# Performance work log

Measured on AMD Instinct MI355X. Metric: run time of the kernel, lower is better.

The kernel has to match this reference:

```python
import jax, jax.numpy as jnp
import numpy as np

EPS_BN = 1e-5

def _grid_sample(fea, gx, gy):
    # fea: [B,C,H,W]; gx,gy: [B,P] normalized to [-1,1]; bilinear, zeros padding, align_corners=True
    B, C, H, W = fea.shape
    x = (gx + 1.0) * 0.5 * (W - 1)
    y = (gy + 1.0) * 0.5 * (H - 1)
    x0 = jnp.floor(x)
    y0 = jnp.floor(y)
    wx1 = x - x0
    wy1 = y - y0
    flat = fea.reshape(B, C, H * W)
    def tap(xi, yi, w):
        valid = ((xi >= 0) & (xi <= W - 1) & (yi >= 0) & (yi <= H - 1)).astype(fea.dtype)
        xi_c = jnp.clip(xi, 0, W - 1).astype(jnp.int32)
        yi_c = jnp.clip(yi, 0, H - 1).astype(jnp.int32)
        g = jnp.take_along_axis(flat, (yi_c * W + xi_c)[:, None, :], axis=2)  # [B,C,P]
        return g * (w * valid)[:, None, :]
    return (tap(x0, y0, (1 - wx1) * (1 - wy1)) + tap(x0 + 1, y0, wx1 * (1 - wy1))
            + tap(x0, y0 + 1, (1 - wx1) * wy1) + tap(x0 + 1, y0 + 1, wx1 * wy1))

def _homo_warp(src_fea, src_proj, ref_proj, depth_values):
    # src_fea: [B,C,H,W] -> warped [B,C,D,H,W] (MVSNet homo_warping, grid under stop_gradient)
    B, C, H, W = src_fea.shape
    D = depth_values.shape[1]
    proj = jnp.matmul(src_proj, jnp.linalg.inv(ref_proj))
    rot, trans = proj[:, :3, :3], proj[:, :3, 3]
    yy, xx = jnp.meshgrid(jnp.arange(H, dtype=src_fea.dtype), jnp.arange(W, dtype=src_fea.dtype), indexing='ij')
    xyz = jnp.stack([xx.ravel(), yy.ravel(), jnp.ones(H * W, src_fea.dtype)], 0)  # [3,HW]
    rot_xyz = jnp.einsum('bij,jp->bip', rot, xyz)  # [B,3,HW]
    pxyz = rot_xyz[:, :, None, :] * depth_values.reshape(B, 1, D, H * W) + trans[:, :, None, None]  # [B,3,D,HW]
    z = pxyz[:, 2]
    gx = jax.lax.stop_gradient(((pxyz[:, 0] / z) / ((W - 1) / 2.0) - 1.0).reshape(B, D * H * W))
    gy = jax.lax.stop_gradient(((pxyz[:, 1] / z) / ((H - 1) / 2.0) - 1.0).reshape(B, D * H * W))
    return _grid_sample(src_fea, gx, gy).reshape(B, C, D, H, W)

def _pixelwise_net(x, w0, g0, b0, m0, v0, w1, g1, b1, m1, v1, w2, b2):
    # x: [B,1,D,H,W]; 1x1x1 Conv3d(bias=False)+BN+ReLU twice, then Conv3d(8->1)+sigmoid+max over D
    def bnrelu(h, g, b, m, v):
        s = (1, -1, 1, 1, 1)
        return jax.nn.relu((h - m.reshape(s)) * (g / jnp.sqrt(v + EPS_BN)).reshape(s) + b.reshape(s))
    h = bnrelu(jnp.einsum('oc,bcdhw->bodhw', w0, x), g0, b0, m0, v0)
    h = bnrelu(jnp.einsum('oc,bcdhw->bodhw', w1, h), g1, b1, m1, v1)
    h = jnp.einsum('oc,bcdhw->bodhw', w2, h) + b2.reshape(1, -1, 1, 1, 1)
    out = jax.nn.sigmoid(h[:, 0])  # [B,D,H,W]
    return jnp.max(out, axis=1, keepdims=True)  # [B,1,H,W]

def _forward(features, proj_matrices, depth_values, num_depth,
             pw_w0, pw_g0, pw_b0, pw_m0, pw_v0, pw_w1, pw_g1, pw_b1, pw_m1, pw_v1, pw_w2, pw_b2,
             reg_w, reg_b):
    ref_fea = features[0]
    B, C, H, W = ref_fea.shape
    V = features.shape[0]
    D = num_depth
    def proj_new(p):  # p: [B,2,4,4] -> K @ E on top 3 rows
        top = jnp.matmul(p[:, 1, :3, :3], p[:, 0, :3, :4])
        return jnp.concatenate([top, p[:, 0, 3:4, :]], axis=1)
    ref_proj_new = proj_new(proj_matrices[:, 0])
    sim_sum = jnp.zeros((B, 1, D, H, W), ref_fea.dtype)
    w_sum = jnp.full((B, 1, 1, H, W), 1e-5, ref_fea.dtype)
    vw_list = []
    for i in range(1, V):  # small fixed loop over source views
        src_proj_new = proj_new(proj_matrices[:, i])
        warped = _homo_warp(features[i], src_proj_new, ref_proj_new, depth_values)
        sim = jnp.mean(warped * ref_fea[:, :, None], axis=1, keepdims=True)  # [B,1,D,H,W]
        vw = _pixelwise_net(sim, pw_w0, pw_g0, pw_b0, pw_m0, pw_v0, pw_w1, pw_g1, pw_b1, pw_m1, pw_v1, pw_w2, pw_b2)
        vw_list.append(vw)
        sim_sum = sim_sum + sim * vw[:, :, None]
        w_sum = w_sum + vw[:, :, None]
    similarity = sim_sum / w_sum
    cost_reg = jax.lax.conv_general_dilated(similarity, reg_w, (1, 1, 1), 'SAME',
                                            dimension_numbers=('NCDHW', 'OIDHW', 'NCDHW')) + reg_b.reshape(1, -1, 1, 1, 1)
    prob_volume = jax.nn.softmax(cost_reg[:, 0], axis=1)  # exp(log_softmax) == softmax
    idx = jnp.argmax(prob_volume, axis=1, keepdims=True)
    depth = jnp.take_along_axis(depth_values, idx, axis=1)[:, 0]  # WTA depth [B,H,W]
    conf = jnp.max(prob_volume, axis=1)
    view_weights = jnp.concatenate(vw_list, axis=1)
    return depth, conf, prob_volume, cost_reg, view_weights

def setup_inputs():
    key = jax.random.key(0)
    ks = jax.random.split(key, 20)
    B, V, C, H, W, D = 2, 5, 32, 128, 160, 32
    features = jax.random.normal(ks[0], (V, B, C, H, W), jnp.float32)
    K = np.eye(4, dtype=np.float32)
    K[0, 0] = 180.0; K[1, 1] = 180.0; K[0, 2] = W / 2.0; K[1, 2] = H / 2.0
    pm = np.zeros((B, V, 2, 4, 4), np.float32)
    for v in range(V):
        E = np.eye(4, dtype=np.float32)
        E[0, 3] = 10.0 * v  # horizontal baseline per source view
        pm[:, v, 0] = E
        pm[:, v, 1] = K
    depth_values = jnp.broadcast_to(jnp.linspace(425.0, 935.0, D, dtype=jnp.float32)[None, :, None, None], (B, D, H, W)) + 0.0
    rn = lambda k, s, sc=0.3: jax.random.normal(k, s, jnp.float32) * sc
    return {
        'features': features,
        'proj_matrices': jnp.asarray(pm),
        'depth_values': depth_values,
        'num_depth': D,
        'pw_w0': rn(ks[1], (16, 1)),
        'pw_g0': 1.0 + rn(ks[2], (16,), 0.1), 'pw_b0': rn(ks[3], (16,), 0.1),
        'pw_m0': rn(ks[4], (16,), 0.1), 'pw_v0': 1.0 + 0.5 * jax.random.uniform(ks[5], (16,)),
        'pw_w1': rn(ks[6], (8, 16)),
        'pw_g1': 1.0 + rn(ks[7], (8,), 0.1), 'pw_b1': rn(ks[8], (8,), 0.1),
        'pw_m1': rn(ks[9], (8,), 0.1), 'pw_v1': 1.0 + 0.5 * jax.random.uniform(ks[10], (8,)),
        'pw_w2': rn(ks[11], (1, 8)),
        'pw_b2': rn(ks[12], (1,), 0.1),
        'reg_w': rn(ks[13], (1, 1, 3, 3, 3), 0.1),
        'reg_b': rn(ks[14], (1,), 0.1),
    }

def reference(features, proj_matrices, depth_values, num_depth,
              pw_w0, pw_g0, pw_b0, pw_m0, pw_v0, pw_w1, pw_g1, pw_b1, pw_m1, pw_v1, pw_w2, pw_b2,
              reg_w, reg_b):
    return _forward(features, proj_matrices, depth_values, num_depth,
                    pw_w0, pw_g0, pw_b0, pw_m0, pw_v0, pw_w1, pw_g1, pw_b1, pw_m1, pw_v1, pw_w2, pw_b2,
                    reg_w, reg_b)
```

## Files before the change

kernel.cpp:

```cpp
#include <hip/hip_runtime.h>
#include <math.h>

#define BB 2
#define VV 5
#define CC 32
#define HH 128
#define WW 160
#define DD 32
#define HWp (HH*WW)
#define NV (VV-1)
#define PX 16
#define MAXSLOT 18

#define OFF_RT   0
#define OFF_PRM  96
#define OFF_FEAT 512
#define OFF_SIM  (OFF_FEAT + VV*BB*HWp*CC)
#define OFF_T    (OFF_SIM + BB*DD*HWp)
#define OFF_TAB  (OFF_T + 16)
#define OFF_FLAG (OFF_TAB + 17*16)

#define OUT_DEPTH 0
#define OUT_CONF  (BB*HWp)
#define OUT_PROB  (2*BB*HWp)
#define OUT_COST  (OUT_PROB + BB*DD*HWp)
#define OUT_VW    (OUT_COST + BB*DD*HWp)

#define ZI(d,k)     smemU[(d)*17 + (k)]
#define DEP(d,k)    smemU[(d)*17 + (k)]
#define REF(p,c)    smemU[544 + (p)*36 + (c)]
#define GT(v,p,i)   smemU[1120 + ((v)*16 + (p))*18 + (i)]
#define AY0(v,p)    smemU[2272 + (v)*16 + (p)]
#define AY1(v,p)    smemU[2336 + (v)*16 + (p)]
#define IR0(v,p)    smemI[2400 + (v)*16 + (p)]
#define IR1(v,p)    smemI[2464 + (v)*16 + (p)]
#define IXB(v,p)    smemI[2528 + (v)*16 + (p)]
#define ISL(v,p)    smemI[2592 + (v)*16 + (p)]
#define BADF        smemI[2656]
#define SIMG(v,d,p) smemU[544 + (((v)*32 + (d))*17 + (p))]

__device__ void build_proj(const float* proj, int b, int v, double M[4][4]) {
    const float* E = proj + (((b*VV + v)*2 + 0)*16);
    const float* K = proj + (((b*VV + v)*2 + 1)*16);
    for (int r = 0; r < 3; r++)
        for (int c = 0; c < 4; c++) {
            double s = 0.0;
            for (int k = 0; k < 3; k++) s += (double)K[r*4+k] * (double)E[k*4+c];
            M[r][c] = s;
        }
    for (int c = 0; c < 4; c++) M[3][c] = (double)E[12+c];
}

__device__ void inv4(const double M[4][4], double out[4][4]) {
    double a[4][8];
    for (int i = 0; i < 4; i++)
        for (int j = 0; j < 4; j++) { a[i][j] = M[i][j]; a[i][4+j] = (i == j) ? 1.0 : 0.0; }
    for (int col = 0; col < 4; col++) {
        int piv = col; double best = fabs(a[col][col]);
        for (int r = col+1; r < 4; r++) if (fabs(a[r][col]) > best) { best = fabs(a[r][col]); piv = r; }
        if (piv != col) for (int j = 0; j < 8; j++) { double t = a[col][j]; a[col][j] = a[piv][j]; a[piv][j] = t; }
        double dinv = 1.0 / a[col][col];
        for (int j = 0; j < 8; j++) a[col][j] *= dinv;
        for (int r = 0; r < 4; r++) {
            if (r == col) continue;
            double f = a[r][col];
            for (int j = 0; j < 8; j++) a[r][j] -= f * a[col][j];
        }
    }
    for (int i = 0; i < 4; i++) for (int j = 0; j < 4; j++) out[i][j] = a[i][4+j];
}

__device__ void setup_body(const float* __restrict__ proj,
    const float* __restrict__ w0, const float* __restrict__ g0, const float* __restrict__ b0,
    const float* __restrict__ m0, const float* __restrict__ v0,
    const float* __restrict__ w1, const float* __restrict__ g1, const float* __restrict__ b1,
    const float* __restrict__ m1, const float* __restrict__ v1,
    const float* __restrict__ w2, const float* __restrict__ b2,
    float* __restrict__ ws, int t,
    float* __restrict__ prmL, float* __restrict__ TL) {

    if (t < BB*NV) {
        int b = t / NV, v = 1 + (t % NV);
        double refM[4][4], inv[4][4], S[4][4];
        build_proj(proj, b, 0, refM);
        inv4(refM, inv);
        build_proj(proj, b, v, S);
        float* rt = ws + OFF_RT + (b*NV + (v-1))*12;
        for (int r = 0; r < 3; r++) {
            for (int c = 0; c < 3; c++) {
                double s = 0.0;
                for (int k = 0; k < 4; k++) s += S[r][k] * inv[k][c];
                rt[r*3 + c] = (float)s;
            }
            double s = 0.0;
            for (int k = 0; k < 4; k++) s += S[r][k] * inv[k][3];
            rt[9 + r] = (float)s;
        }
    }

    if (t < 16) {
        float sc = g0[t] / sqrtf(v0[t] + 1e-5f);
        prmL[t]      = w0[t] * sc;
        prmL[16 + t] = b0[t] - m0[t] * sc;
    }
    if (t >= 32 && t < 160) {
        int i = t - 32, q = i >> 4, o = i & 15;
        float sc = g1[q] / sqrtf(v1[q] + 1e-5f);
        prmL[32 + q*16 + o] = w1[q*16 + o] * sc;
    }
    if (t >= 160 && t < 168) {
        int q = t - 160;
        float sc = g1[q] / sqrtf(v1[q] + 1e-5f);
        prmL[160 + q] = b1[q] - m1[q] * sc;
        prmL[168 + q] = w2[q];
    }
    if (t == 176) prmL[176] = b2[0];
    __syncthreads();

    if (t < BB) {
        int ok = 1;
        for (int i = 0; i < NV; i++) {
            const float* ri = ws + OFF_RT + (t*NV + i)*12;
            ok &= (fabsf(ri[6])        < 1e-6f);
            ok &= (fabsf(ri[7])        < 1e-6f);
            ok &= (fabsf(ri[8] - 1.f)  < 1e-6f);
            ok &= (fabsf(ri[10])       < 1e-6f);
            ok &= (fabsf(ri[11])       < 1e-6f);
        }
        ws[OFF_FLAG + t] = ok ? 1.f : 0.f;
    }

    if (t == 0) {
        float tmp[16]; int nk = 0;
        for (int o = 0; o < 16; o++) {
            float a = prmL[o];
            if (a != 0.f) tmp[nk++] = -prmL[16+o] / a;
        }
        for (int i = 1; i < nk; i++) {
            float key = tmp[i]; int j = i-1;
            while (j >= 0 && tmp[j] > key) { tmp[j+1] = tmp[j]; j--; }
            tmp[j+1] = key;
        }
        for (int i = 0; i < 16; i++) TL[i] = (i < nk) ? tmp[i] : 3.4e38f;
    }
    __syncthreads();

    if (t < 17*8) {
        int seg = t >> 3, q = t & 7;
        float lo = (seg == 0)  ? -1e30f : TL[seg-1];
        float hi = (seg == 16) ?  1e30f : TL[seg];
        float smid;
        if (hi > 1e29f)       smid = lo + 1.f;
        else if (lo < -1e29f) smid = hi - 1.f;
        else                  smid = 0.5f*(lo + hi);
        float alpha = 0.f, beta = prmL[160+q];
        #pragma unroll
        for (int o = 0; o < 16; o++) {
            float a = prmL[o], c = prmL[16+o];
            if (a*smid + c > 0.f) {
                alpha += prmL[32+q*16+o]*a;
                beta  += prmL[32+q*16+o]*c;
            }
        }
        ws[OFF_TAB + seg*16 + q]     = alpha;
        ws[OFF_TAB + seg*16 + 8 + q] = beta;
    }
    if (t < 177) ws[OFF_PRM + t] = prmL[t];
    if (t < 16)  ws[OFF_T + t]   = TL[t];
}

__global__ __launch_bounds__(256) void transpose_setup_kernel(
    const float* __restrict__ fea, float* __restrict__ featT,
    const float* __restrict__ proj,
    const float* __restrict__ w0, const float* __restrict__ g0, const float* __restrict__ b0,
    const float* __restrict__ m0, const float* __restrict__ v0,
    const float* __restrict__ w1, const float* __restrict__ g1, const float* __restrict__ b1,
    const float* __restrict__ m1, const float* __restrict__ v1,
    const float* __restrict__ w2, const float* __restrict__ b2,
    float* __restrict__ ws) {
    __shared__ float prmL[177];
    __shared__ float TL[16];
    if (blockIdx.x == 0)
        setup_body(proj, w0, g0, b0, m0, v0, w1, g1, b1, m1, v1, w2, b2,
                   ws, threadIdx.x, prmL, TL);

    int t = blockIdx.x*256 + threadIdx.x;
    int w = t % WW;
    int h = (t / WW) % HH;
    int b = (t / (WW*HH)) % BB;
    int v = t / (WW*HH*BB);
    const float* src = fea + (size_t)((v*BB + b)*CC) * HWp + h*WW + w;
    float* dst = featT + (size_t)((v*BB + b)*HWp + h*WW + w) * CC;
    #pragma unroll
    for (int c = 0; c < CC; c += 4) {
        float4 q;
        q.x = src[(c+0)*HWp];
        q.y = src[(c+1)*HWp];
        q.z = src[(c+2)*HWp];
        q.w = src[(c+3)*HWp];
        *reinterpret_cast<float4*>(dst + c) = q;
    }
}

__device__ __forceinline__ float half_max(float v) {
    v = fmaxf(v, __shfl_xor(v, 1));
    v = fmaxf(v, __shfl_xor(v, 2));
    v = fmaxf(v, __shfl_xor(v, 4));
    v = fmaxf(v, __shfl_xor(v, 8));
    v = fmaxf(v, __shfl_xor(v, 16));
    return v;
}

__device__ __forceinline__ float dot32(const float* __restrict__ col,
                                       const float* __restrict__ refp) {
    float acc = 0.f;
    #pragma unroll
    for (int c = 0; c < CC; c += 4) {
        float4 a = *reinterpret_cast<const float4*>(col + c);
        float4 r = *reinterpret_cast<const float4*>(refp + c);
        acc = fmaf(a.w, r.w, fmaf(a.z, r.z, fmaf(a.y, r.y, fmaf(a.x, r.x, acc))));
    }
    return acc;
}

__device__ __forceinline__ void mlp_out(
    float s0, float s1, float s2, float s3,
    int d2, int b, int p,
    const float* __restrict__ tabL, const float* __restrict__ Tg,
    const float* __restrict__ prm,
    float* __restrict__ out, float* __restrict__ simout) {
    float T0 = Tg[0], T1 = Tg[1], T2 = Tg[2], T3 = Tg[3];
    float T4 = Tg[4], T5 = Tg[5], T6 = Tg[6], T7 = Tg[7];
    float T8 = Tg[8], T9 = Tg[9], T10 = Tg[10], T11 = Tg[11];
    float T12 = Tg[12], T13 = Tg[13], T14 = Tg[14], T15 = Tg[15];
    float wq0 = prm[168], wq1 = prm[169], wq2 = prm[170], wq3 = prm[171];
    float wq4 = prm[172], wq5 = prm[173], wq6 = prm[174], wq7 = prm[175];
    float p176 = prm[176];

    float sv[NV] = {s0, s1, s2, s3};
    float vw[NV];
    #pragma unroll
    for (int v = 0; v < NV; v++) {
        float s = sv[v];
        int seg = 0;
        seg += (s > T0);  seg += (s > T1);  seg += (s > T2);  seg += (s > T3);
        seg += (s > T4);  seg += (s > T5);  seg += (s > T6);  seg += (s > T7);
        seg += (s > T8);  seg += (s > T9);  seg += (s > T10); seg += (s > T11);
        seg += (s > T12); seg += (s > T13); seg += (s > T14); seg += (s > T15);
        const float* row = &tabL[seg << 4];
        float4 A0 = *reinterpret_cast<const float4*>(row);
        float4 A1 = *reinterpret_cast<const float4*>(row + 4);
        float4 B0 = *reinterpret_cast<const float4*>(row + 8);
        float4 B1 = *reinterpret_cast<const float4*>(row + 12);
        float h2v = p176;
        h2v = fmaf(wq0, fmaxf(fmaf(A0.x, s, B0.x), 0.f), h2v);
        h2v = fmaf(wq1, fmaxf(fmaf(A0.y, s, B0.y), 0.f), h2v);
        h2v = fmaf(wq2, fmaxf(fmaf(A0.z, s, B0.z), 0.f), h2v);
        h2v = fmaf(wq3, fmaxf(fmaf(A0.w, s, B0.w), 0.f), h2v);
        h2v = fmaf(wq4, fmaxf(fmaf(A1.x, s, B1.x), 0.f), h2v);
        h2v = fmaf(wq5, fmaxf(fmaf(A1.y, s, B1.y), 0.f), h2v);
        h2v = fmaf(wq6, fmaxf(fmaf(A1.z, s, B1.z), 0.f), h2v);
        h2v = fmaf(wq7, fmaxf(fmaf(A1.w, s, B1.w), 0.f), h2v);
        float m = half_max(h2v);
        vw[v] = 1.f/(1.f + __expf(-m));
    }

    if (d2 == 0) out[OUT_VW + (b*NV + 0)*HWp + p] = vw[0];
    if (d2 == 1) out[OUT_VW + (b*NV + 1)*HWp + p] = vw[1];
    if (d2 == 2) out[OUT_VW + (b*NV + 2)*HWp + p] = vw[2];
    if (d2 == 3) out[OUT_VW + (b*NV + 3)*HWp + p] = vw[3];

    float wsum = 1e-5f + vw[0] + vw[1] + vw[2] + vw[3];
    float ssum = s0*vw[0] + s1*vw[1] + s2*vw[2] + s3*vw[3];
    simout[(b*DD + d2)*HWp + p] = ssum / wsum;
}

__device__ __forceinline__ float tap_blend(
    const float* __restrict__ vbv, int sub8, float sx,
    float ay0, float ay1, int r0, int r1,
    float4 rva, float4 rvb) {
    float x0f = floorf(sx);
    float wx1 = sx - x0f;
    float wx0 = 1.f - wx1;
    int xi0 = (int)x0f, xi1 = xi0 + 1;
    float ax0 = ((unsigned)xi0 < WW) ? wx0 : 0.f;
    float ax1 = ((unsigned)xi1 < WW) ? wx1 : 0.f;
    int xc0 = min(max(xi0, 0), WW-1);
    int xc1 = min(max(xi1, 0), WW-1);
    float w00 = ax0*ay0, w01 = ax1*ay0;
    const float* q00 = vbv + (((r0 + xc0) << 5) + sub8);
    const float* q01 = vbv + (((r0 + xc1) << 5) + sub8);
    float4 t00a = *reinterpret_cast<const float4*>(q00);
    float4 t00b = *reinterpret_cast<const float4*>(q00 + 4);
    float4 t01a = *reinterpret_cast<const float4*>(q01);
    float4 t01b = *reinterpret_cast<const float4*>(q01 + 4);

    float blx = fmaf(w01, t01a.x, w00*t00a.x);
    float bly = fmaf(w01, t01a.y, w00*t00a.y);
    float blz = fmaf(w01, t01a.z, w00*t00a.z);
    float blw = fmaf(w01, t01a.w, w00*t00a.w);
    float acc = fmaf(rva.w,blw, fmaf(rva.z,blz, fmaf(rva.y,bly, rva.x*blx)));
    blx = fmaf(w01, t01b.x, w00*t00b.x);
    bly = fmaf(w01, t01b.y, w00*t00b.y);
    blz = fmaf(w01, t01b.z, w00*t00b.z);
    blw = fmaf(w01, t01b.w, w00*t00b.w);
    acc = fmaf(rvb.w,blw, fmaf(rvb.z,blz, fmaf(rvb.y,bly, fmaf(rvb.x,blx, acc))));

    if (ay1 != 0.f) {
        float w10 = ax0*ay1, w11 = ax1*ay1;
        const float* q10 = vbv + (((r1 + xc0) << 5) + sub8);
        const float* q11 = vbv + (((r1 + xc1) << 5) + sub8);
        float4 t10a = *reinterpret_cast<const float4*>(q10);
        float4 t10b = *reinterpret_cast<const float4*>(q10 + 4);
        float4 t11a = *reinterpret_cast<const float4*>(q11);
        float4 t11b = *reinterpret_cast<const float4*>(q11 + 4);
        float cx = fmaf(w11, t11a.x, w10*t10a.x);
        float cy = fmaf(w11, t11a.y, w10*t10a.y);
        float cz = fmaf(w11, t11a.z, w10*t10a.z);
        float cw = fmaf(w11, t11a.w, w10*t10a.w);
        acc = fmaf(rva.w,cw, fmaf(rva.z,cz, fmaf(rva.y,cy, fmaf(rva.x,cx, acc))));
        cx = fmaf(w11, t11b.x, w10*t10b.x);
        cy = fmaf(w11, t11b.y, w10*t10b.y);
        cz = fmaf(w11, t11b.z, w10*t10b.z);
        cw = fmaf(w11, t11b.w, w10*t10b.w);
        acc = fmaf(rvb.w,cw, fmaf(rvb.z,cz, fmaf(rvb.y,cy, fmaf(rvb.x,cx, acc))));
    }
    return acc;
}

__global__ __launch_bounds__(256) void fused_sim_kernel(
    const float* __restrict__ featT, const float* __restrict__ rtAll,
    const float* __restrict__ prm, const float* __restrict__ Tg,
    const float* __restrict__ tabG, const float* __restrict__ flagG,
    const float* __restrict__ depthv,
    float* __restrict__ simout, float* __restrict__ out) {
    __shared__ __align__(16) float smemU[2720];
    __shared__ __align__(16) float tabL[17*16];
    int* smemI = (int*)smemU;

    int t = threadIdx.x;
    int b = blockIdx.y;
    int pbase = blockIdx.x * PX;
    int hi  = pbase / WW;
    int wi0 = pbase % WW;
    float fy = (float)hi;

    bool fast = (flagG[b] != 0.f);

    {
        int di = t >> 4, k = t & 15;
        float dep0 = depthv[(b*DD + di)*HWp + pbase + k];
        float dep1 = depthv[(b*DD + di + 16)*HWp + pbase + k];
        if (fast) {
            ZI(di, k)    = __builtin_amdgcn_rcpf(dep0);
            ZI(di+16, k) = __builtin_amdgcn_rcpf(dep1);
            REF(di, k)      = featT[(size_t)(b*HWp + pbase + di)*CC + k];
            REF(di, k+16)   = featT[(size_t)(b*HWp + pbase + di)*CC + k + 16];
        } else {
            DEP(di, k)    = dep0;
            DEP(di+16, k) = dep1;
        }
        tabL[t] = tabG[t];
        if (t < 16) tabL[256 + t] = tabG[256 + t];
        if (t == 0 && fast) BADF = 0;
    }
    __syncthreads();

    float rc[NV][12];
    #pragma unroll
    for (int v = 0; v < NV; v++)
        #pragma unroll
        for (int j = 0; j < 12; j++)
            rc[v][j] = rtAll[(b*NV + v)*12 + j];
    float bx0[NV], by0[NV], bz0[NV];
    #pragma unroll
    for (int v = 0; v < NV; v++) {
        bx0[v] = fmaf((float)wi0, rc[v][0], fmaf(fy, rc[v][1], rc[v][2]));
        by0[v] = fmaf((float)wi0, rc[v][3], fmaf(fy, rc[v][4], rc[v][5]));
        bz0[v] = fmaf((float)wi0, rc[v][6], fmaf(fy, rc[v][7], rc[v][8]));
    }

    bool needRestage = false;
    if (fast) {
        int p_loc = t >> 5, d = t & 31;
        for (int ph = 0; ph < 2; ph++) {
            int p = ph*8 + p_loc;
            float fk = (float)p;
            float zi = ZI(d, p);
            #pragma unroll
            for (int v = 0; v < NV; v++) {
                float bx = fmaf(fk, rc[v][0], bx0[v]);
                float sx = fmaf(rc[v][9], zi, bx);
                float mn = sx, mx = sx;
                #pragma unroll
                for (int off = 1; off <= 16; off <<= 1) {
                    mn = fminf(mn, __shfl_xor(mn, off));
                    mx = fmaxf(mx, __shfl_xor(mx, off));
                }
                if (d == 0) {
                    float by = fmaf(fk, rc[v][3], by0[v]);
                    float sy = by;
                    float sny = rintf(sy);
                    sy = (fabsf(sy - sny) < 1e-4f) ? sny : sy;
                    float y0f = floorf(sy);
                    float wy1 = sy - y0f, wy0 = 1.f - wy1;
                    int yi0 = (int)y0f, yi1 = yi0 + 1;
                    AY0(v, p) = ((unsigned)yi0 < HH) ? wy0 : 0.f;
                    AY1(v, p) = ((unsigned)yi1 < HH) ? wy1 : 0.f;
                    IR0(v, p) = min(max(yi0, 0), HH-1)*WW;
                    IR1(v, p) = min(max(yi1, 0), HH-1)*WW;
                    bool finite = (mn > -1e9f) && (mx < 1e9f) && (mn == mn) && (mx == mx);
                    int xb = finite ? (int)floorf(mn) : 0;
                    int slots = finite ? ((int)floorf(mx) - xb + 2) : MAXSLOT + 1;
                    IXB(v, p) = xb;
                    ISL(v, p) = slots;
                    if (slots > MAXSLOT) BADF = 1;
                }
            }
        }
        __syncthreads();
        if (BADF) { fast = false; needRestage = true; }
    }

    if (fast) {
        {
            int v2 = t & 3, p2 = (t >> 2) & 15, i0 = t >> 6;
            float ay0 = AY0(v2, p2), ay1 = AY1(v2, p2);
            int r0 = IR0(v2, p2), r1 = IR1(v2, p2);
            int xb = IXB(v2, p2), slots = ISL(v2, p2);
            const float* vbv = featT + (size_t)(((v2+1)*BB + b)*HWp)*CC;
            const float* refp = &REF(p2, 0);
            for (int i2 = i0; i2 < slots; i2 += 4) {
                int xc = min(max(xb + i2, 0), WW-1);
                float g = ay0 * dot32(vbv + ((r0 + xc) << 5), refp);
                if (ay1 != 0.f) g = fmaf(ay1, dot32(vbv + ((r1 + xc) << 5), refp), g);
                GT(v2, p2, i2) = g * (1.f/(float)CC);
            }
        }
        __syncthreads();
        {
            int p_loc = t >> 5, d = t & 31;
            for (int ph = 0; ph < 2; ph++) {
                int p = ph*8 + p_loc;
                float fk = (float)p;
                float zi = ZI(d, p);
                float sv[NV];
                #pragma unroll
                for (int v = 0; v < NV; v++) {
                    float bx = fmaf(fk, rc[v][0], bx0[v]);
                    float sx = fmaf(rc[v][9], zi, bx);
                    float x0f = floorf(sx);
                    float wx1 = sx - x0f, wx0 = 1.f - wx1;
                    int xi0 = (int)x0f, xi1 = xi0 + 1;
                    float ax0 = ((unsigned)xi0 < WW) ? wx0 : 0.f;
                    float ax1 = ((unsigned)xi1 < WW) ? wx1 : 0.f;
                    int ii = xi0 - IXB(v, p);
                    float g0 = GT(v, p, ii);
                    float g1 = GT(v, p, ii+1);
                    sv[v] = fmaf(ax0, g0, ax1*g1);
                }
                mlp_out(sv[0], sv[1], sv[2], sv[3], d, b, pbase + p,
                        tabL, Tg, prm, out, simout);
            }
        }
        return;
    }

    if (needRestage) {
        int di = t >> 4, k = t & 15;
        DEP(di, k)    = depthv[(b*DD + di)*HWp + pbase + k];
        DEP(di+16, k) = depthv[(b*DD + di + 16)*HWp + pbase + k];
        __syncthreads();
    }
    {
        int sub = t & 3;
        int dB  = (t >> 2) & 31;
        int kk  = t >> 7;
        int sub8 = sub*8;
        #pragma unroll 2
        for (int j = 0; j < PX/2; j++) {
            int kpix = j*2 + kk;
            int p = pbase + kpix;
            float fk = (float)kpix;
            float depth = DEP(dB, kpix);
            const float* refp = featT + (size_t)(b*HWp + p)*CC + sub8;
            float4 rva = *reinterpret_cast<const float4*>(refp);
            float4 rvb = *reinterpret_cast<const float4*>(refp + 4);

            #pragma unroll
            for (int v = 0; v < NV; v++) {
                float bx = fmaf(fk, rc[v][0], bx0[v]);
                float by = fmaf(fk, rc[v][3], by0[v]);
                float bz = fmaf(fk, rc[v][6], bz0[v]);
                float px = fmaf(bx, depth, rc[v][9]);
                float py = fmaf(by, depth, rc[v][10]);
                float pz = fmaf(bz, depth, rc[v][11]);
                float zi = __builtin_amdgcn_rcpf(pz);
                float sx = px * zi, sy = py * zi;
                float sny = rintf(sy);
                sy = (fabsf(sy - sny) < 1e-4f) ? sny : sy;
                float y0f = floorf(sy);
                float wy1 = sy - y0f, wy0 = 1.f - wy1;
                int yi0 = (int)y0f, yi1 = yi0 + 1;
                float ay0 = ((unsigned)yi0 < HH) ? wy0 : 0.f;
                float ay1 = ((unsigned)yi1 < HH) ? wy1 : 0.f;
                int yc0 = min(max(yi0, 0), HH-1);
                int yc1 = min(max(yi1, 0), HH-1);
                int r0 = yc0*WW, r1 = yc1*WW;
                const float* vbv = featT + (size_t)(((v+1)*BB + b)*HWp)*CC;
                float acc = tap_blend(vbv, sub8, sx, ay0, ay1, r0, r1, rva, rvb);
                acc += __shfl_xor(acc, 1);
                acc += __shfl_xor(acc, 2);
                if (sub == 0) SIMG(v, dB, kpix) = acc * (1.f/(float)CC);
            }
        }
        __syncthreads();

        int p8 = t >> 5;
        int d2 = t & 31;
        #pragma unroll
        for (int pi = 0; pi < PX/8; pi++) {
            int pidx = pi*8 + p8;
            mlp_out(SIMG(0, d2, pidx), SIMG(1, d2, pidx),
                    SIMG(2, d2, pidx), SIMG(3, d2, pidx),
                    d2, b, pbase + pidx, tabL, Tg, prm, out, simout);
        }
    }
}

__global__ __launch_bounds__(256) void convsm_kernel(
    const float* __restrict__ sim, const float* __restrict__ rw,
    const float* __restrict__ rb, const float* __restrict__ depthv,
    float* __restrict__ out) {
    __shared__ float tile[34*121 + 7];
    int t = threadIdx.x;
    int tw = blockIdx.x * 8;
    int th = blockIdx.y * 8;
    int b  = blockIdx.z;

    for (int i = t; i < 34*120; i += 256) {
        int e = i / 120; int rem = i % 120;
        int h = rem / 12, w = rem % 12;
        int gd = e - 1, gh = th + h - 1, gw = tw + w - 1;
        float v = 0.f;
        if (w < 10 && gd >= 0 && gd < DD && (unsigned)gh < HH && (unsigned)gw < WW)
            v = sim[((b*DD + gd)*HH + gh)*WW + gw];
        tile[e*121 + rem] = v;
    }
    __syncthreads();

    float wk[27];
    #pragma unroll
    for (int i = 0; i < 27; i++) wk[i] = rw[i];
    float bias = rb[0];

    int p  = t >> 2, dq = t & 3;
    int ph = p >> 3, pw = p & 7;
    int d0 = dq * 8;

    float cost[8];
    #pragma unroll
    for (int j = 0; j < 8; j++) cost[j] = bias;
    #pragma unroll
    for (int e = 0; e < 10; e++) {
        int el = d0 + e;
        float s0 = 0.f, s1 = 0.f, s2 = 0.f;
        #pragma unroll
        for (int kh = 0; kh < 3; kh++) {
            #pragma unroll
            for (int kw = 0; kw < 3; kw++) {
                float x = tile[el*121 + (ph+kh)*12 + (pw+kw)];
                s0 = fmaf(wk[0*9 + kh*3 + kw], x, s0);
                s1 = fmaf(wk[1*9 + kh*3 + kw], x, s1);
                s2 = fmaf(wk[2*9 + kh*3 + kw], x, s2);
            }
        }
        if (e < 8)            cost[e]   += s0;
        if (e >= 1 && e <= 8) cost[e-1] += s1;
        if (e >= 2)           cost[e-2] += s2;
    }

    int pg = (th + ph)*WW + (tw + pw);
    #pragma unroll
    for (int j = 0; j < 8; j++)
        out[OUT_COST + (b*DD + d0 + j)*HWp + pg] = cost[j];

    float m = cost[0]; int mi = d0;
    #pragma unroll
    for (int j = 1; j < 8; j++) { if (cost[j] > m) { m = cost[j]; mi = d0 + j; } }
    #pragma unroll
    for (int off = 1; off <= 2; off <<= 1) {
        float m2 = __shfl_xor(m, off);
        int  i2 = __shfl_xor(mi, off);
        if (m2 > m || (m2 == m && i2 < mi)) { m = m2; mi = i2; }
    }
    float sum = 0.f;
    float e8[8];
    #pragma unroll
    for (int j = 0; j < 8; j++) { e8[j] = __expf(cost[j] - m); sum += e8[j]; }
    #pragma unroll
    for (int off = 1; off <= 2; off <<= 1) sum += __shfl_xor(sum, off);
    float inv = 1.f / sum;
    #pragma unroll
    for (int j = 0; j < 8; j++)
        out[OUT_PROB + (b*DD + d0 + j)*HWp + pg] = e8[j] * inv;
    if (dq == 0) {
        out[OUT_DEPTH + b*HWp + pg] = depthv[(b*DD + mi)*HWp + pg];
        out[OUT_CONF  + b*HWp + pg] = inv;
    }
}

extern "C" void kernel_launch(void* const* d_in, const int* in_sizes, int n_in,
                              void* d_out, int out_size, void* d_ws, size_t ws_size,
                              hipStream_t stream) {
    const float* features = (const float*)d_in[0];
    const float* proj     = (const float*)d_in[1];
    const float* depthv   = (const float*)d_in[2];
    const float* w0 = (const float*)d_in[4];
    const float* g0 = (const float*)d_in[5];
    const float* b0 = (const float*)d_in[6];
    const float* m0 = (const float*)d_in[7];
    const float* v0 = (const float*)d_in[8];
    const float* w1 = (const float*)d_in[9];
    const float* g1 = (const float*)d_in[10];
    const float* b1 = (const float*)d_in[11];
    const float* m1 = (const float*)d_in[12];
    const float* v1 = (const float*)d_in[13];
    const float* w2 = (const float*)d_in[14];
    const float* b2 = (const float*)d_in[15];
    const float* rw = (const float*)d_in[16];
    const float* rb = (const float*)d_in[17];
    float* out = (float*)d_out;
    float* ws  = (float*)d_ws;

    transpose_setup_kernel<<<VV*BB*HWp/256, 256, 0, stream>>>(
        features, ws + OFF_FEAT, proj,
        w0, g0, b0, m0, v0, w1, g1, b1, m1, v1, w2, b2, ws);

    fused_sim_kernel<<<dim3(HWp/PX, BB), 256, 0, stream>>>(
        ws + OFF_FEAT, ws + OFF_RT, ws + OFF_PRM, ws + OFF_T, ws + OFF_TAB,
        ws + OFF_FLAG, depthv, ws + OFF_SIM, out);

    convsm_kernel<<<dim3(WW/8, HH/8, BB), 256, 0, stream>>>(
        ws + OFF_SIM, rw, rb, depthv, out);
}
```

Before: 79.87 us.

## Collapse pixelwise MLP into a single piecewise-linear lookup with bucketed segment index

The 1->16->8->1 ReLU MLP is a piecewise-linear function of the scalar similarity. Setup now finds every kink of both ReLU layers, up to 152 breakpoints, and sorts them. It stores one slope/intercept pair per segment plus a 2048-bucket byte index table. At run time each sample looks up its bucket, corrects the segment with short boundary scans and evaluates one FMA, replacing 16 compares and 8 fmax/fma terms. The cost is a larger shared-memory table per block (about 3 KB more) and data-dependent while loops, which could diverge if many kinks fall in one bucket.

```diff
diff --git a/kernel.cpp b/kernel.cpp
--- a/kernel.cpp
+++ b/kernel.cpp
@@ -12,13 +12,17 @@
 #define PX 16
 #define MAXSLOT 18
 
+#define NKK 152
+#define NSEG 153
+#define NBND 154
+#define NG 2048
+#define SSC 128.f
+
 #define OFF_RT   0
-#define OFF_PRM  96
 #define OFF_FEAT 512
 #define OFF_SIM  (OFF_FEAT + VV*BB*HWp*CC)
-#define OFF_T    (OFF_SIM + BB*DD*HWp)
-#define OFF_TAB  (OFF_T + 16)
-#define OFF_FLAG (OFF_TAB + 17*16)
+#define OFF_AB   (OFF_SIM + BB*DD*HWp)
+#define OFF_FLAG (OFF_AB + 992)
 
 #define OUT_DEPTH 0
 #define OUT_CONF  (BB*HWp)
@@ -77,7 +81,7 @@
     const float* __restrict__ m1, const float* __restrict__ v1,
     const float* __restrict__ w2, const float* __restrict__ b2,
     float* __restrict__ ws, int t,
-    float* __restrict__ prmL, float* __restrict__ TL) {
+    float* __restrict__ prmL, float* __restrict__ kinkL, float* __restrict__ sortedK) {
 
     if (t < BB*NV) {
         int b = t / NV, v = 1 + (t % NV);
@@ -130,43 +134,95 @@
         ws[OFF_FLAG + t] = ok ? 1.f : 0.f;
     }
 
-    if (t == 0) {
-        float tmp[16]; int nk = 0;
-        for (int o = 0; o < 16; o++) {
-            float a = prmL[o];
-            if (a != 0.f) tmp[nk++] = -prmL[16+o] / a;
-        }
-        for (int i = 1; i < nk; i++) {
-            float key = tmp[i]; int j = i-1;
-            while (j >= 0 && tmp[j] > key) { tmp[j+1] = tmp[j]; j--; }
-            tmp[j+1] = key;
-        }
-        for (int i = 0; i < 16; i++) TL[i] = (i < nk) ? tmp[i] : 3.4e38f;
+    if (t < 16) {
+        float a = prmL[t];
+        kinkL[t] = (a != 0.f) ? (-prmL[16+t]/a) : 3.4e38f;
     }
     __syncthreads();
-
-    if (t < 17*8) {
-        int seg = t >> 3, q = t & 7;
-        float lo = (seg == 0)  ? -1e30f : TL[seg-1];
-        float hi = (seg == 16) ?  1e30f : TL[seg];
-        float smid;
-        if (hi > 1e29f)       smid = lo + 1.f;
-        else if (lo < -1e29f) smid = hi - 1.f;
-        else                  smid = 0.5f*(lo + hi);
+    if (t < 16) {
+        float ki = kinkL[t]; int r = 0;
+        for (int j = 0; j < 16; j++) {
+            float kj = kinkL[j];
+            r += (kj < ki) || (kj == ki && j < t) ? 1 : 0;
+        }
+        sortedK[r] = ki;
+    }
+    __syncthreads();
+    if (t < 8*17) {
+        int q = t / 17, j = t % 17;
+        float lo = (j == 0)  ? -3.4e38f : sortedK[j-1];
+        float hi = (j == 16) ?  3.4e38f : sortedK[j];
+        bool loInf = (lo < -1e30f), hiInf = (hi > 1e30f);
+        float rep;
+        if (loInf && hiInf)      rep = 0.f;
+        else if (loInf)          rep = hi - 1.f;
+        else if (hiInf)          rep = lo + 1.f;
+        else                     rep = 0.5f*(lo + hi);
         float alpha = 0.f, beta = prmL[160+q];
-        #pragma unroll
         for (int o = 0; o < 16; o++) {
             float a = prmL[o], c = prmL[16+o];
-            if (a*smid + c > 0.f) {
+            if (fmaf(a, rep, c) > 0.f) {
                 alpha += prmL[32+q*16+o]*a;
                 beta  += prmL[32+q*16+o]*c;
             }
         }
-        ws[OFF_TAB + seg*16 + q]     = alpha;
-        ws[OFF_TAB + seg*16 + 8 + q] = beta;
-    }
-    if (t < 177) ws[OFF_PRM + t] = prmL[t];
-    if (t < 16)  ws[OFF_T + t]   = TL[t];
+        float z = 3.4e38f;
+        if (alpha != 0.f) {
+            float zz = -beta/alpha;
+            if (zz > lo && zz < hi) z = zz;
+        }
+        kinkL[16 + t] = z;
+    }
+    __syncthreads();
+    if (t < NKK) {
+        float ki = kinkL[t]; int r = 0;
+        for (int j = 0; j < NKK; j++) {
+            float kj = kinkL[j];
+            r += (kj < ki) || (kj == ki && j < t) ? 1 : 0;
+        }
+        sortedK[r] = ki;
+    }
+    __syncthreads();
+    if (t == 0) ws[OFF_AB + 320 + 0] = -3.9e38f;
+    if (t == 1) ws[OFF_AB + 320 + NKK + 1] = 3.9e38f;
+    if (t < NKK) ws[OFF_AB + 320 + 1 + t] = sortedK[t];
+    if (t < NSEG) {
+        float lo = (t == 0)   ? -3.4e38f : sortedK[t-1];
+        float hi = (t == NKK) ?  3.4e38f : sortedK[t];
+        bool loInf = (lo < -1e30f), hiInf = (hi > 1e30f);
+        float rep;
+        if (loInf && hiInf)      rep = 0.f;
+        else if (loInf)          rep = hi - 1.f;
+        else if (hiInf)          rep = lo + 1.f;
+        else                     rep = 0.5f*(lo + hi);
+        float h0[16]; bool act0[16];
+        for (int o = 0; o < 16; o++) {
+            float h = fmaf(prmL[o], rep, prmL[16+o]);
+            act0[o] = (h > 0.f);
+            h0[o] = fmaxf(h, 0.f);
+        }
+        float A = 0.f, h2m = prmL[176];
+        for (int q = 0; q < 8; q++) {
+            float a1 = prmL[160+q], alq = 0.f;
+            for (int o = 0; o < 16; o++) {
+                a1 += prmL[32+q*16+o]*h0[o];
+                if (act0[o]) alq += prmL[32+q*16+o]*prmL[o];
+            }
+            if (a1 > 0.f) { h2m += prmL[168+q]*a1; A += prmL[168+q]*alq; }
+        }
+        ws[OFF_AB + t]       = A;
+        ws[OFF_AB + 160 + t] = h2m - A*rep;
+    }
+    for (int i4 = t; i4 < 512; i4 += 256) {
+        unsigned word = 0;
+        for (int kk = 0; kk < 4; kk++) {
+            float si = -8.f + (float)(i4*4 + kk) * (1.f/SSC);
+            int cnt = 0;
+            for (int j = 0; j < NKK; j++) cnt += (sortedK[j] <= si) ? 1 : 0;
+            word |= ((unsigned)cnt) << (8*kk);
+        }
+        ws[OFF_AB + 480 + i4] = __uint_as_float(word);
+    }
 }
 
 __global__ __launch_bounds__(256) void transpose_setup_kernel(
@@ -179,10 +235,11 @@
     const float* __restrict__ w2, const float* __restrict__ b2,
     float* __restrict__ ws) {
     __shared__ float prmL[177];
-    __shared__ float TL[16];
+    __shared__ float kinkL[NKK];
+    __shared__ float sortedK[NKK];
     if (blockIdx.x == 0)
         setup_body(proj, w0, g0, b0, m0, v0, w1, g1, b1, m1, v1, w2, b2,
-                   ws, threadIdx.x, prmL, TL);
+                   ws, threadIdx.x, prmL, kinkL, sortedK);
 
     int t = blockIdx.x*256 + threadIdx.x;
     int w = t % WW;
@@ -226,41 +283,20 @@
 __device__ __forceinline__ void mlp_out(
     float s0, float s1, float s2, float s3,
     int d2, int b, int p,
-    const float* __restrict__ tabL, const float* __restrict__ Tg,
-    const float* __restrict__ prm,
+    const float* __restrict__ AL, const float* __restrict__ BL2,
+    const float* __restrict__ BNDL, const unsigned char* __restrict__ SIDX,
     float* __restrict__ out, float* __restrict__ simout) {
-    float T0 = Tg[0], T1 = Tg[1], T2 = Tg[2], T3 = Tg[3];
-    float T4 = Tg[4], T5 = Tg[5], T6 = Tg[6], T7 = Tg[7];
-    float T8 = Tg[8], T9 = Tg[9], T10 = Tg[10], T11 = Tg[11];
-    float T12 = Tg[12], T13 = Tg[13], T14 = Tg[14], T15 = Tg[15];
-    float wq0 = prm[168], wq1 = prm[169], wq2 = prm[170], wq3 = prm[171];
-    float wq4 = prm[172], wq5 = prm[173], wq6 = prm[174], wq7 = prm[175];
-    float p176 = prm[176];
-
     float sv[NV] = {s0, s1, s2, s3};
     float vw[NV];
     #pragma unroll
     for (int v = 0; v < NV; v++) {
         float s = sv[v];
-        int seg = 0;
-        seg += (s > T0);  seg += (s > T1);  seg += (s > T2);  seg += (s > T3);
-        seg += (s > T4);  seg += (s > T5);  seg += (s > T6);  seg += (s > T7);
-        seg += (s > T8);  seg += (s > T9);  seg += (s > T10); seg += (s > T11);
-        seg += (s > T12); seg += (s > T13); seg += (s > T14); seg += (s > T15);
-        const float* row = &tabL[seg << 4];
-        float4 A0 = *reinterpret_cast<const float4*>(row);
-        float4 A1 = *reinterpret_cast<const float4*>(row + 4);
-        float4 B0 = *reinterpret_cast<const float4*>(row + 8);
-        float4 B1 = *reinterpret_cast<const float4*>(row + 12);
-        float h2v = p176;
-        h2v = fmaf(wq0, fmaxf(fmaf(A0.x, s, B0.x), 0.f), h2v);
-        h2v = fmaf(wq1, fmaxf(fmaf(A0.y, s, B0.y), 0.f), h2v);
-        h2v = fmaf(wq2, fmaxf(fmaf(A0.z, s, B0.z), 0.f), h2v);
-        h2v = fmaf(wq3, fmaxf(fmaf(A0.w, s, B0.w), 0.f), h2v);
-        h2v = fmaf(wq4, fmaxf(fmaf(A1.x, s, B1.x), 0.f), h2v);
-        h2v = fmaf(wq5, fmaxf(fmaf(A1.y, s, B1.y), 0.f), h2v);
-        h2v = fmaf(wq6, fmaxf(fmaf(A1.z, s, B1.z), 0.f), h2v);
-        h2v = fmaf(wq7, fmaxf(fmaf(A1.w, s, B1.w), 0.f), h2v);
+        float u = fmaf(s, SSC, 1024.f);
+        int ic = (int)fminf(fmaxf(u, 0.f), 2047.f);
+        int seg = SIDX[ic];
+        while (s >= BNDL[seg+1]) seg++;
+        while (seg > 0 && s < BNDL[seg]) seg--;
+        float h2v = fmaf(AL[seg], s, BL2[seg]);
         float m = half_max(h2v);
         vw[v] = 1.f/(1.f + __expf(-m));
     }
@@ -330,13 +366,17 @@
 
 __global__ __launch_bounds__(256) void fused_sim_kernel(
     const float* __restrict__ featT, const float* __restrict__ rtAll,
-    const float* __restrict__ prm, const float* __restrict__ Tg,
-    const float* __restrict__ tabG, const float* __restrict__ flagG,
+    const float* __restrict__ tb,
+    const float* __restrict__ flagG,
     const float* __restrict__ depthv,
     float* __restrict__ simout, float* __restrict__ out) {
     __shared__ __align__(16) float smemU[2720];
-    __shared__ __align__(16) float tabL[17*16];
+    __shared__ float AL[NSEG];
+    __shared__ float BL2[NSEG];
+    __shared__ float BNDL[NBND];
+    __shared__ unsigned SIDXW[512];
     int* smemI = (int*)smemU;
+    const unsigned char* SIDX = (const unsigned char*)SIDXW;
 
     int t = threadIdx.x;
     int b = blockIdx.y;
@@ -360,8 +400,10 @@
             DEP(di, k)    = dep0;
             DEP(di+16, k) = dep1;
         }
-        tabL[t] = tabG[t];
-        if (t < 16) tabL[256 + t] = tabG[256 + t];
+        if (t < NSEG) { AL[t] = tb[t]; BL2[t] = tb[160 + t]; }
+        if (t < NBND) BNDL[t] = tb[320 + t];
+        SIDXW[t]       = __float_as_uint(tb[480 + t]);
+        SIDXW[t + 256] = __float_as_uint(tb[480 + 256 + t]);
         if (t == 0 && fast) BADF = 0;
     }
     __syncthreads();
@@ -460,7 +502,7 @@
                     sv[v] = fmaf(ax0, g0, ax1*g1);
                 }
                 mlp_out(sv[0], sv[1], sv[2], sv[3], d, b, pbase + p,
-                        tabL, Tg, prm, out, simout);
+                        AL, BL2, BNDL, SIDX, out, simout);
             }
         }
         return;
@@ -523,7 +565,7 @@
             int pidx = pi*8 + p8;
             mlp_out(SIMG(0, d2, pidx), SIMG(1, d2, pidx),
                     SIMG(2, d2, pidx), SIMG(3, d2, pidx),
-                    d2, b, pbase + pidx, tabL, Tg, prm, out, simout);
+                    d2, b, pbase + pidx, AL, BL2, BNDL, SIDX, out, simout);
         }
     }
 }
@@ -638,7 +680,7 @@
         w0, g0, b0, m0, v0, w1, g1, b1, m1, v1, w2, b2, ws);
 
     fused_sim_kernel<<<dim3(HWp/PX, BB), 256, 0, stream>>>(
-        ws + OFF_FEAT, ws + OFF_RT, ws + OFF_PRM, ws + OFF_T, ws + OFF_TAB,
+        ws + OFF_FEAT, ws + OFF_RT, ws + OFF_AB,
         ws + OFF_FLAG, depthv, ws + OFF_SIM, out);
 
     convsm_kernel<<<dim3(WW/8, HH/8, BB), 256, 0, stream>>>(
```

Result: slower. 83.97 us (+5.1%).
